# Kernel tuning notes

Measured on AMD Instinct MI355X. Metric: run time of the kernel, lower is better.

## Reference

```python
import jax, jax.numpy as jnp
import numpy as np

T, B, D, H, S = 512, 32, 1024, 1024, 512


def setup_inputs() -> dict:
    key = jax.random.key(0)
    ks = jax.random.split(key, 10)
    sc = 0.02
    return {
        "x": jax.random.normal(ks[0], (T, B, D), jnp.float32),
        "h0": jax.random.normal(ks[1], (B, H), jnp.float32),
        "c0": jax.random.normal(ks[2], (B, H), jnp.float32),
        "ctx": jax.random.normal(ks[3], (S, B, H), jnp.float32),
        # nn.Linear(input_size, 4*hidden_size) with bias
        "W_ih": jax.random.normal(ks[4], (4 * H, D), jnp.float32) * sc,
        "b_ih": jax.random.normal(ks[5], (4 * H,), jnp.float32) * sc,
        # nn.Linear(hidden_size, 4*hidden_size) with bias
        "W_hh": jax.random.normal(ks[6], (4 * H, H), jnp.float32) * sc,
        "b_hh": jax.random.normal(ks[7], (4 * H,), jnp.float32) * sc,
        # SoftDotAttention: linear_in (H->H, no bias), linear_out (2H->H, no bias)
        "W_in": jax.random.normal(ks[8], (H, H), jnp.float32) * sc,
        "W_out": jax.random.normal(ks[9], (H, 2 * H), jnp.float32) * sc,
    }


def reference(x, h0, c0, ctx, W_ih, b_ih, W_hh, b_hh, W_in, W_out):
    ctx_b = jnp.swapaxes(ctx, 0, 1)  # [B, S, H] (ctx.transpose(0,1))

    def step(carry, xt):
        hx, cx = carry
        gates = xt @ W_ih.T + b_ih + hx @ W_hh.T + b_hh  # [B, 4H]
        i, f, g, o = jnp.split(gates, 4, axis=1)
        cy = jax.nn.sigmoid(f) * cx + jax.nn.sigmoid(i) * jnp.tanh(g)
        hy = jax.nn.sigmoid(o) * jnp.tanh(cy)  # [B, H]
        # SoftDotAttention
        target = hy @ W_in.T  # [B, H]
        attn = jax.nn.softmax(jnp.einsum("bsh,bh->bs", ctx_b, target), axis=-1)
        wc = jnp.einsum("bs,bsh->bh", attn, ctx_b)  # weighted context
        h_tilde = jnp.tanh(jnp.concatenate([wc, hy], axis=1) @ W_out.T)
        return (h_tilde, cy), h_tilde

    (hT, cT), out = jax.lax.scan(step, (h0, c0), x)
    return out, hT, cT
```

## Files before the change

### kernel.cpp

```cpp
#include <hip/hip_runtime.h>
#include <hip/hip_bf16.h>
#include <cstdint>
#include <cstddef>

#define TT 512
#define BB 32
#define DD 1024
#define HH 1024
#define SS 512

typedef _Float16 f16x8 __attribute__((ext_vector_type(8)));
typedef _Float16 f16x4 __attribute__((ext_vector_type(4)));
typedef _Float16 f16x2 __attribute__((ext_vector_type(2)));
typedef float f32x4 __attribute__((ext_vector_type(4)));

__device__ __forceinline__ float sigm(float x) { return 1.0f / (1.0f + __expf(-x)); }
__device__ __forceinline__ float tanh_fast(float x) {
    return 1.0f - 2.0f / (__expf(2.0f * x) + 1.0f);
}
__device__ __forceinline__ f16x8 cvt8(const float* __restrict__ p) {
    float4 u = *(const float4*)p;
    float4 v = *(const float4*)(p + 4);
    f16x8 r;
    r[0] = (_Float16)u.x; r[1] = (_Float16)u.y; r[2] = (_Float16)u.z; r[3] = (_Float16)u.w;
    r[4] = (_Float16)v.x; r[5] = (_Float16)v.y; r[6] = (_Float16)v.z; r[7] = (_Float16)v.w;
    return r;
}

__device__ __forceinline__ void st_u32_coh(unsigned* p, unsigned v) {
    __hip_atomic_store(p, v, __ATOMIC_RELAXED, __HIP_MEMORY_SCOPE_AGENT);
}
__device__ __forceinline__ unsigned ld_u32_coh(const unsigned* p) {
    return __hip_atomic_load(p, __ATOMIC_RELAXED, __HIP_MEMORY_SCOPE_AGENT);
}
__device__ __forceinline__ f16x8 ld16_coh(const _Float16* p) {
    union { unsigned long long q[2]; f16x8 h; } u;
    u.q[0] = __hip_atomic_load((const unsigned long long*)p, __ATOMIC_RELAXED,
                               __HIP_MEMORY_SCOPE_AGENT);
    u.q[1] = __hip_atomic_load((const unsigned long long*)p + 1, __ATOMIC_RELAXED,
                               __HIP_MEMORY_SCOPE_AGENT);
    return u.h;
}

__global__ __launch_bounds__(256) void k_cvt(const float* __restrict__ s,
                                             _Float16* __restrict__ d, int n4) {
    for (int i = blockIdx.x * blockDim.x + threadIdx.x; i < n4; i += gridDim.x * blockDim.x) {
        float4 v = ((const float4*)s)[i];
        f16x4 h;
        h[0] = (_Float16)v.x; h[1] = (_Float16)v.y;
        h[2] = (_Float16)v.z; h[3] = (_Float16)v.w;
        ((f16x4*)d)[i] = h;
    }
}

__global__ void k_bias(const float* __restrict__ bih, const float* __restrict__ bhh,
                       float* __restrict__ bsum) {
    const int i = blockIdx.x * blockDim.x + threadIdx.x;
    if (i < 4 * HH) bsum[i] = bih[i] + bhh[i];
}

__global__ void k_init(const float* __restrict__ c0, float* __restrict__ cbuf) {
    const int i = blockIdx.x * blockDim.x + threadIdx.x;
    if (i < BB * HH) cbuf[i] = c0[i];
}

__global__ void k_zero(unsigned* __restrict__ p) {
    if (threadIdx.x == 0 && blockIdx.x == 0) *p = 0u;
}

__global__ void k_fin(const float* __restrict__ lasth, const float* __restrict__ cbuf,
                      float* __restrict__ hT, float* __restrict__ cT) {
    const int i = blockIdx.x * blockDim.x + threadIdx.x;
    if (i < BB * HH) {
        hT[i] = lasth[i];
        cT[i] = cbuf[i];
    }
}

__global__ __launch_bounds__(256) void k_pre(const float* __restrict__ x,
                                             const float* __restrict__ Wih,
                                             _Float16* __restrict__ gx) {
    const int wave = (blockIdx.x * blockDim.x + threadIdx.x) >> 6;
    const int lane = threadIdx.x & 63;
    const int m0 = (wave >> 6) * 64, n0 = (wave & 63) * 64;
    const int lm = lane & 15, q8 = (lane >> 4) * 8;

    f32x4 acc[4][4];
    #pragma unroll
    for (int i = 0; i < 4; ++i)
        #pragma unroll
        for (int j = 0; j < 4; ++j) acc[i][j] = (f32x4)0.0f;

    for (int k0 = 0; k0 < DD; k0 += 32) {
        f16x8 a[4], b[4];
        #pragma unroll
        for (int i = 0; i < 4; ++i)
            a[i] = cvt8(x + (size_t)(m0 + i * 16 + lm) * DD + k0 + q8);
        #pragma unroll
        for (int j = 0; j < 4; ++j)
            b[j] = cvt8(Wih + (size_t)(n0 + j * 16 + lm) * DD + k0 + q8);
        #pragma unroll
        for (int i = 0; i < 4; ++i)
            #pragma unroll
            for (int j = 0; j < 4; ++j)
                acc[i][j] = __builtin_amdgcn_mfma_f32_16x16x32_f16(a[i], b[j], acc[i][j], 0, 0, 0);
    }
    const int rq = (lane >> 4) * 4;
    #pragma unroll
    for (int i = 0; i < 4; ++i)
        #pragma unroll
        for (int j = 0; j < 4; ++j)
            #pragma unroll
            for (int r = 0; r < 4; ++r)
                gx[(size_t)(m0 + i * 16 + rq + r) * (4 * HH) + n0 + j * 16 + lm] =
                    (_Float16)acc[i][j][r];
}

__global__ __launch_bounds__(256) void k_trwin(const float* __restrict__ Win,
                                               _Float16* __restrict__ WinT) {
    __shared__ float tile[32][33];
    const int bx = blockIdx.x & 31, by = blockIdx.x >> 5;
    const int tx = threadIdx.x & 31, ty = threadIdx.x >> 5;
    #pragma unroll
    for (int r = 0; r < 4; ++r)
        tile[ty + r * 8][tx] = Win[(size_t)(by * 32 + ty + r * 8) * HH + bx * 32 + tx];
    __syncthreads();
    #pragma unroll
    for (int r = 0; r < 4; ++r)
        WinT[(size_t)(bx * 32 + ty + r * 8) * HH + by * 32 + tx] =
            (_Float16)tile[tx][ty + r * 8];
}

__global__ __launch_bounds__(256) void k_ctxw(const float* __restrict__ ctxf,
                                              const _Float16* __restrict__ WinT,
                                              _Float16* __restrict__ ctxW) {
    const int wave = (blockIdx.x * blockDim.x + threadIdx.x) >> 6;
    const int lane = threadIdx.x & 63;
    const int m0 = (wave >> 4) * 64, n0 = (wave & 15) * 64;
    const int lm = lane & 15, q8 = (lane >> 4) * 8;

    f32x4 acc[4][4];
    #pragma unroll
    for (int i = 0; i < 4; ++i)
        #pragma unroll
        for (int j = 0; j < 4; ++j) acc[i][j] = (f32x4)0.0f;

    for (int k0 = 0; k0 < HH; k0 += 32) {
        f16x8 a[4], b[4];
        #pragma unroll
        for (int i = 0; i < 4; ++i)
            a[i] = cvt8(ctxf + (size_t)(m0 + i * 16 + lm) * HH + k0 + q8);
        #pragma unroll
        for (int j = 0; j < 4; ++j)
            b[j] = *(const f16x8*)(WinT + (size_t)(n0 + j * 16 + lm) * HH + k0 + q8);
        #pragma unroll
        for (int i = 0; i < 4; ++i)
            #pragma unroll
            for (int j = 0; j < 4; ++j)
                acc[i][j] = __builtin_amdgcn_mfma_f32_16x16x32_f16(a[i], b[j], acc[i][j], 0, 0, 0);
    }
    const int rq = (lane >> 4) * 4;
    #pragma unroll
    for (int i = 0; i < 4; ++i)
        #pragma unroll
        for (int j = 0; j < 4; ++j)
            #pragma unroll
            for (int r = 0; r < 4; ++r)
                ctxW[(size_t)(m0 + i * 16 + rq + r) * HH + n0 + j * 16 + lm] =
                    (_Float16)acc[i][j][r];
}

__device__ __forceinline__ void gbar(unsigned* __restrict__ cnt, unsigned target) {
    __syncthreads();
    if (threadIdx.x == 0) {
        asm volatile("s_waitcnt vmcnt(0)" ::: "memory");
        __hip_atomic_fetch_add(cnt, 1u, __ATOMIC_RELAXED, __HIP_MEMORY_SCOPE_AGENT);
        int guard = 0;
        while (__hip_atomic_load(cnt, __ATOMIC_RELAXED, __HIP_MEMORY_SCOPE_AGENT) < target) {
            __builtin_amdgcn_s_sleep(2);
            if (++guard > (1 << 22)) break;
        }
    }
    __syncthreads();
}

__global__ __launch_bounds__(512, 1) void k_persist(
    const _Float16* __restrict__ x16,
    const _Float16* __restrict__ ctx_h,
    const _Float16* __restrict__ ctxW,
    const float* __restrict__ Whh,
    const float* __restrict__ Wih,
    const float* __restrict__ Wout,
    const float* __restrict__ bsum,
    float* __restrict__ cbuf,
    _Float16* __restrict__ h16,
    _Float16* __restrict__ hy16,
    _Float16* __restrict__ wc16,
    float* __restrict__ scores,
    float* __restrict__ out,
    unsigned* __restrict__ bar) {
    __shared__ __align__(16) _Float16 sWHH[16 * 1024];
    __shared__ __align__(16) _Float16 sWIH[16 * 1024];
    __shared__ __align__(16) _Float16 sWOUT[16 * 2048];
    __shared__ __align__(16) float sRED[4096];
    __shared__ float sSM[512];

    const int bid = blockIdx.x;
    const int tid = threadIdx.x;
    const int w = tid >> 6, lane = tid & 63;
    const int lm = lane & 15, q8 = (lane >> 4) * 8;
    const int j0 = bid * 4;
    const int n0 = bid * 16;

    for (int idx = tid; idx < 16 * 128; idx += 512) {
        const int p = idx >> 7, k8 = idx & 127;
        const int g = (p >> 2) * HH + j0 + (p & 3);
        const int dst = (p * 2048 + k8 * 16) ^ ((p & 7) << 4);
        *(f16x8*)((char*)sWHH + dst) = cvt8(Whh + (size_t)g * HH + k8 * 8);
        *(f16x8*)((char*)sWIH + dst) = cvt8(Wih + (size_t)g * DD + k8 * 8);
    }
    if (bid < 64) {
        for (int idx = tid; idx < 16 * 256; idx += 512) {
            const int p = idx >> 8, k8 = idx & 255;
            *(f16x8*)((char*)sWOUT + ((p * 4096 + k8 * 16) ^ ((p & 7) << 4))) =
                cvt8(Wout + (size_t)(n0 + p) * (2 * HH) + k8 * 8);
        }
    }
    __syncthreads();

    unsigned round = 0;
    for (int t = 0; t < TT; ++t) {
        {
            const int kb = (w & 3) * 256;
            f32x4 acc0 = (f32x4)0.0f, acc1 = (f32x4)0.0f;
            if (w < 4) {
                #pragma unroll
                for (int kk = 0; kk < 256; kk += 32) {
                    const int k0 = kb + kk + q8;
                    f16x8 a0 = ld16_coh(h16 + (size_t)lm * HH + k0);
                    f16x8 a1 = ld16_coh(h16 + (size_t)(16 + lm) * HH + k0);
                    f16x8 bb = *(const f16x8*)((const char*)sWHH +
                                 ((lm * 2048 + k0 * 2) ^ ((lm & 7) << 4)));
                    acc0 = __builtin_amdgcn_mfma_f32_16x16x32_f16(a0, bb, acc0, 0, 0, 0);
                    acc1 = __builtin_amdgcn_mfma_f32_16x16x32_f16(a1, bb, acc1, 0, 0, 0);
                }
            } else {
                const _Float16* Xb = x16 + (size_t)t * (BB * DD);
                #pragma unroll
                for (int kk = 0; kk < 256; kk += 32) {
                    const int k0 = kb + kk + q8;
                    f16x8 a0 = *(const f16x8*)(Xb + (size_t)lm * DD + k0);
                    f16x8 a1 = *(const f16x8*)(Xb + (size_t)(16 + lm) * DD + k0);
                    f16x8 bb = *(const f16x8*)((const char*)sWIH +
                                 ((lm * 2048 + k0 * 2) ^ ((lm & 7) << 4)));
                    acc0 = __builtin_amdgcn_mfma_f32_16x16x32_f16(a0, bb, acc0, 0, 0, 0);
                    acc1 = __builtin_amdgcn_mfma_f32_16x16x32_f16(a1, bb, acc1, 0, 0, 0);
                }
            }
            ((f32x4*)sRED)[(w * 2 + 0) * 64 + lane] = acc0;
            ((f32x4*)sRED)[(w * 2 + 1) * 64 + lane] = acc1;
            __syncthreads();
            {
                const int b = tid >> 4, p = tid & 15;
                const int mt = b >> 4, bi = b & 15;
                const int ln = ((bi >> 2) << 4) | p, r = bi & 3;
                float gv = 0.0f;
                #pragma unroll
                for (int w2 = 0; w2 < 8; ++w2)
                    gv += sRED[((w2 * 2 + mt) * 64 + ln) * 4 + r];
                sSM[tid] = gv;
            }
            __syncthreads();
            if (tid < 64) {
                const int b = tid >> 1, cp = (tid & 1) * 2;
                union { _Float16 h[2]; unsigned u; } pk;
                #pragma unroll
                for (int cc = 0; cc < 2; ++cc) {
                    const int c = cp + cc, j = j0 + c;
                    const float gi = sSM[b * 16 + 0 + c] + bsum[j];
                    const float gf = sSM[b * 16 + 4 + c] + bsum[HH + j];
                    const float gg = sSM[b * 16 + 8 + c] + bsum[2 * HH + j];
                    const float go = sSM[b * 16 + 12 + c] + bsum[3 * HH + j];
                    const float cprev = cbuf[b * HH + j];
                    const float cy = sigm(gf) * cprev + sigm(gi) * tanh_fast(gg);
                    const float hv = sigm(go) * tanh_fast(cy);
                    cbuf[b * HH + j] = cy;
                    pk.h[cc] = (_Float16)hv;
                }
                st_u32_coh((unsigned*)(hy16 + (size_t)b * HH + j0 + cp), pk.u);
            }
        }
        ++round;
        gbar(bar, 256u * round);

        {
            const int b = bid & 31, s0 = (bid >> 5) * 64;
            const _Float16* hrow = hy16 + (size_t)b * HH + lane * 16;
            const f16x8 hv0 = ld16_coh(hrow);
            const f16x8 hv1 = ld16_coh(hrow + 8);
            float hf[16];
            #pragma unroll
            for (int i = 0; i < 8; ++i) { hf[i] = (float)hv0[i]; hf[8 + i] = (float)hv1[i]; }
            #pragma unroll
            for (int i = 0; i < 8; ++i) {
                const int s = s0 + w * 8 + i;
                const _Float16* crow = ctxW + ((size_t)s * BB + b) * HH + lane * 16;
                const f16x8 c0 = *(const f16x8*)(crow);
                const f16x8 c1 = *(const f16x8*)(crow + 8);
                float sum = 0.0f;
                #pragma unroll
                for (int jj = 0; jj < 8; ++jj)
                    sum += hf[jj] * (float)c0[jj] + hf[8 + jj] * (float)c1[jj];
                #pragma unroll
                for (int off = 32; off > 0; off >>= 1) sum += __shfl_down(sum, off, 64);
                if (lane == 0)
                    st_u32_coh((unsigned*)(scores + b * SS + s), __float_as_uint(sum));
            }
        }
        ++round;
        gbar(bar, 256u * round);

        {
            const int b = bid >> 3, h0 = (bid & 7) * 128;
            const float v = __uint_as_float(ld_u32_coh((const unsigned*)(scores + b * SS + tid)));
            float mx = v;
            #pragma unroll
            for (int off = 32; off > 0; off >>= 1) mx = fmaxf(mx, __shfl_xor(mx, off, 64));
            if (lane == 0) sRED[w] = mx;
            __syncthreads();
            mx = sRED[0];
            #pragma unroll
            for (int w2 = 1; w2 < 8; ++w2) mx = fmaxf(mx, sRED[w2]);
            const float e = __expf(v - mx);
            sSM[tid] = e;
            float ssum = e;
            #pragma unroll
            for (int off = 32; off > 0; off >>= 1) ssum += __shfl_xor(ssum, off, 64);
            if (lane == 0) sRED[8 + w] = ssum;
            __syncthreads();
            float tot = 0.0f;
            #pragma unroll
            for (int w2 = 0; w2 < 8; ++w2) tot += sRED[8 + w2];
            const float inv = 1.0f / tot;
            float a0 = 0.0f, a1 = 0.0f;
            const _Float16* cb = ctx_h + ((size_t)(w * 64) * BB + b) * HH + h0 + lane * 2;
            #pragma unroll 8
            for (int i = 0; i < 64; ++i) {
                const float aw = sSM[w * 64 + i];
                const f16x2 u = *(const f16x2*)(cb + (size_t)i * (BB * HH));
                a0 += aw * (float)u[0];
                a1 += aw * (float)u[1];
            }
            __syncthreads();
            sRED[(w * 64 + lane) * 2 + 0] = a0;
            sRED[(w * 64 + lane) * 2 + 1] = a1;
            __syncthreads();
            if (tid < 64) {
                const int ln = tid;
                float sv0 = 0.0f, sv1 = 0.0f;
                #pragma unroll
                for (int w2 = 0; w2 < 8; ++w2) {
                    sv0 += sRED[(w2 * 64 + ln) * 2 + 0];
                    sv1 += sRED[(w2 * 64 + ln) * 2 + 1];
                }
                union { _Float16 h[2]; unsigned u; } pk;
                pk.h[0] = (_Float16)(sv0 * inv);
                pk.h[1] = (_Float16)(sv1 * inv);
                st_u32_coh((unsigned*)(wc16 + (size_t)b * HH + h0 + ln * 2), pk.u);
            }
        }
        ++round;
        gbar(bar, 256u * round);

        if (bid < 64) {
            const _Float16* Ab = (w < 4) ? wc16 : hy16;
            const int kb = (w & 3) * 256;
            const int koff = (w < 4) ? 0 : HH;
            f32x4 acc0 = (f32x4)0.0f, acc1 = (f32x4)0.0f;
            #pragma unroll
            for (int kk = 0; kk < 256; kk += 32) {
                const int k0 = kb + kk + q8;
                f16x8 a0 = ld16_coh(Ab + (size_t)lm * HH + k0);
                f16x8 a1 = ld16_coh(Ab + (size_t)(16 + lm) * HH + k0);
                f16x8 bb = *(const f16x8*)((char*)sWOUT +
                             ((lm * 4096 + (koff + k0) * 2) ^ ((lm & 7) << 4)));
                acc0 = __builtin_amdgcn_mfma_f32_16x16x32_f16(a0, bb, acc0, 0, 0, 0);
                acc1 = __builtin_amdgcn_mfma_f32_16x16x32_f16(a1, bb, acc1, 0, 0, 0);
            }
            ((f32x4*)sRED)[(w * 2 + 0) * 64 + lane] = acc0;
            ((f32x4*)sRED)[(w * 2 + 1) * 64 + lane] = acc1;
            __syncthreads();
            {
                const int b = tid >> 4, p = tid & 15;
                const int mt = b >> 4, bi = b & 15;
                const int ln = ((bi >> 2) << 4) | p, r = bi & 3;
                float v2 = 0.0f;
                #pragma unroll
                for (int w2 = 0; w2 < 8; ++w2)
                    v2 += sRED[((w2 * 2 + mt) * 64 + ln) * 4 + r];
                const float ht = tanh_fast(v2);
                out[(size_t)t * (BB * HH) + b * HH + n0 + p] = ht;
                sSM[tid] = ht;
            }
            __syncthreads();
            if (tid < 256) {
                const int b2 = tid >> 3, pp = (tid & 7) * 2;
                union { _Float16 h[2]; unsigned u; } pk;
                pk.h[0] = (_Float16)sSM[b2 * 16 + pp];
                pk.h[1] = (_Float16)sSM[b2 * 16 + pp + 1];
                st_u32_coh((unsigned*)(h16 + (size_t)b2 * HH + n0 + pp), pk.u);
            }
        }
        ++round;
        gbar(bar, 256u * round);
    }
}

__global__ __launch_bounds__(64) void k_step1(const float* __restrict__ hprev,
                                              const _Float16* __restrict__ Whh_h,
                                              const float* __restrict__ Whh_f,
                                              const _Float16* __restrict__ gx_t,
                                              const float* __restrict__ xt_f,
                                              const _Float16* __restrict__ Wih_h,
                                              const float* __restrict__ Wih_f,
                                              const float* __restrict__ bsum,
                                              float* __restrict__ cbuf,
                                              float* __restrict__ hy,
                                              int use_pre, int staged) {
    const int wave = blockIdx.x;
    const int lane = threadIdx.x;
    const int m0 = (wave >> 6) * 16;
    const int j0 = (wave & 63) * 16;
    const int lm = lane & 15, q8 = (lane >> 4) * 8;

    f32x4 acc[4];
    #pragma unroll
    for (int q = 0; q < 4; ++q) acc[q] = (f32x4)0.0f;

    const float* arow = hprev + (size_t)(m0 + lm) * HH;
    if (staged) {
        for (int k0 = 0; k0 < HH; k0 += 32) {
            f16x8 a = cvt8(arow + k0 + q8);
            #pragma unroll
            for (int q = 0; q < 4; ++q) {
                f16x8 b = *(const f16x8*)(Whh_h + (size_t)(q * HH + j0 + lm) * HH + k0 + q8);
                acc[q] = __builtin_amdgcn_mfma_f32_16x16x32_f16(a, b, acc[q], 0, 0, 0);
            }
        }
    } else {
        for (int k0 = 0; k0 < HH; k0 += 32) {
            f16x8 a = cvt8(arow + k0 + q8);
            #pragma unroll
            for (int q = 0; q < 4; ++q) {
                f16x8 b = cvt8(Whh_f + (size_t)(q * HH + j0 + lm) * HH + k0 + q8);
                acc[q] = __builtin_amdgcn_mfma_f32_16x16x32_f16(a, b, acc[q], 0, 0, 0);
            }
        }
    }
    if (!use_pre) {
        const float* xrow = xt_f + (size_t)(m0 + lm) * DD;
        if (staged) {
            for (int k0 = 0; k0 < DD; k0 += 32) {
                f16x8 a = cvt8(xrow + k0 + q8);
                #pragma unroll
                for (int q = 0; q < 4; ++q) {
                    f16x8 b = *(const f16x8*)(Wih_h + (size_t)(q * HH + j0 + lm) * DD + k0 + q8);
                    acc[q] = __builtin_amdgcn_mfma_f32_16x16x32_f16(a, b, acc[q], 0, 0, 0);
                }
            }
        } else {
            for (int k0 = 0; k0 < DD; k0 += 32) {
                f16x8 a = cvt8(xrow + k0 + q8);
                #pragma unroll
                for (int q = 0; q < 4; ++q) {
                    f16x8 b = cvt8(Wih_f + (size_t)(q * HH + j0 + lm) * DD + k0 + q8);
                    acc[q] = __builtin_amdgcn_mfma_f32_16x16x32_f16(a, b, acc[q], 0, 0, 0);
                }
            }
        }
    }
    const int rq = (lane >> 4) * 4;
    const int j = j0 + lm;
    const float bs_i = bsum[j], bs_f = bsum[HH + j], bs_g = bsum[2 * HH + j], bs_o = bsum[3 * HH + j];
    #pragma unroll
    for (int r = 0; r < 4; ++r) {
        const int b = m0 + rq + r;
        float gi = acc[0][r] + bs_i, gf = acc[1][r] + bs_f;
        float gg = acc[2][r] + bs_g, go = acc[3][r] + bs_o;
        if (use_pre) {
            const _Float16* g = gx_t + (size_t)b * (4 * HH);
            gi += (float)g[j];
            gf += (float)g[HH + j];
            gg += (float)g[2 * HH + j];
            go += (float)g[3 * HH + j];
        }
        const float cprev = cbuf[b * HH + j];
        const float cy = sigm(gf) * cprev + sigm(gi) * tanh_fast(gg);
        const float hv = sigm(go) * tanh_fast(cy);
        cbuf[b * HH + j] = cy;
        hy[b * HH + j] = hv;
    }
}

__global__ __launch_bounds__(64) void k_target(const float* __restrict__ hy,
                                               const _Float16* __restrict__ Win_h,
                                               const float* __restrict__ Win_f,
                                               float* __restrict__ target,
                                               int staged) {
    const int wave = blockIdx.x;
    const int lane = threadIdx.x;
    const int m0 = (wave >> 6) * 16;
    const int j0 = (wave & 63) * 16;
    const int lm = lane & 15, q8 = (lane >> 4) * 8;

    f32x4 acc = (f32x4)0.0f;
    const float* arow = hy + (size_t)(m0 + lm) * HH;
    if (staged) {
        for (int k0 = 0; k0 < HH; k0 += 32) {
            f16x8 a = cvt8(arow + k0 + q8);
            f16x8 b = *(const f16x8*)(Win_h + (size_t)(j0 + lm) * HH + k0 + q8);
            acc = __builtin_amdgcn_mfma_f32_16x16x32_f16(a, b, acc, 0, 0, 0);
        }
    } else {
        for (int k0 = 0; k0 < HH; k0 += 32) {
            f16x8 a = cvt8(arow + k0 + q8);
            f16x8 b = cvt8(Win_f + (size_t)(j0 + lm) * HH + k0 + q8);
            acc = __builtin_amdgcn_mfma_f32_16x16x32_f16(a, b, acc, 0, 0, 0);
        }
    }
    const int rq = (lane >> 4) * 4;
    const int j = j0 + lm;
    #pragma unroll
    for (int r = 0; r < 4; ++r)
        target[(m0 + rq + r) * HH + j] = acc[r];
}

__global__ __launch_bounds__(256) void k_scores(const _Float16* __restrict__ ctx_h,
                                                const float* __restrict__ ctx_f,
                                                const float* __restrict__ target,
                                                float* __restrict__ scores, int staged) {
    const int idx = (blockIdx.x * blockDim.x + threadIdx.x) >> 6;
    const int lane = threadIdx.x & 63;
    const int b = idx >> 9;
    const int s = idx & 511;
    const float* trow = target + b * HH + lane * 16;
    float4 t0 = *(const float4*)(trow);
    float4 t1 = *(const float4*)(trow + 4);
    float4 t2 = *(const float4*)(trow + 8);
    float4 t3 = *(const float4*)(trow + 12);
    float sum = 0.0f;
    if (staged) {
        const _Float16* crow = ctx_h + ((size_t)s * BB + b) * HH + lane * 16;
        f16x8 c0 = *(const f16x8*)(crow);
        f16x8 c1 = *(const f16x8*)(crow + 8);
        sum += (float)c0[0] * t0.x + (float)c0[1] * t0.y + (float)c0[2] * t0.z + (float)c0[3] * t0.w;
        sum += (float)c0[4] * t1.x + (float)c0[5] * t1.y + (float)c0[6] * t1.z + (float)c0[7] * t1.w;
        sum += (float)c1[0] * t2.x + (float)c1[1] * t2.y + (float)c1[2] * t2.z + (float)c1[3] * t2.w;
        sum += (float)c1[4] * t3.x + (float)c1[5] * t3.y + (float)c1[6] * t3.z + (float)c1[7] * t3.w;
    } else {
        const float* crow = ctx_f + ((size_t)s * BB + b) * HH + lane * 16;
        float4 c0 = *(const float4*)(crow);
        float4 c1 = *(const float4*)(crow + 4);
        float4 c2 = *(const float4*)(crow + 8);
        float4 c3 = *(const float4*)(crow + 12);
        sum += c0.x * t0.x + c0.y * t0.y + c0.z * t0.z + c0.w * t0.w;
        sum += c1.x * t1.x + c1.y * t1.y + c1.z * t1.z + c1.w * t1.w;
        sum += c2.x * t2.x + c2.y * t2.y + c2.z * t2.z + c2.w * t2.w;
        sum += c3.x * t3.x + c3.y * t3.y + c3.z * t3.z + c3.w * t3.w;
    }
    #pragma unroll
    for (int off = 32; off > 0; off >>= 1) sum += __shfl_down(sum, off, 64);
    if (lane == 0) scores[b * SS + s] = sum;
}

__global__ __launch_bounds__(256) void k_attn(const _Float16* __restrict__ ctx_h,
                                              const float* __restrict__ ctx_f,
                                              const float* __restrict__ scores,
                                              float* __restrict__ wc, int staged) {
    __shared__ float sm[SS];
    __shared__ float red[256];
    const int b = blockIdx.x >> 1;
    const int hc = blockIdx.x & 1;
    const int t = threadIdx.x;

    const float v0 = scores[b * SS + t];
    const float v1 = scores[b * SS + 256 + t];
    red[t] = fmaxf(v0, v1);
    __syncthreads();
    for (int o = 128; o > 0; o >>= 1) {
        if (t < o) red[t] = fmaxf(red[t], red[t + o]);
        __syncthreads();
    }
    const float mx = red[0];
    __syncthreads();
    const float e0 = __expf(v0 - mx);
    const float e1 = __expf(v1 - mx);
    sm[t] = e0;
    sm[t + 256] = e1;
    red[t] = e0 + e1;
    __syncthreads();
    for (int o = 128; o > 0; o >>= 1) {
        if (t < o) red[t] += red[t + o];
        __syncthreads();
    }
    const float inv = 1.0f / red[0];

    const int h = hc * 512 + t * 2;
    float a0 = 0.0f, a1 = 0.0f;
    if (staged) {
        const _Float16* cbase = ctx_h + (size_t)b * HH + h;
        #pragma unroll 8
        for (int s = 0; s < SS; ++s) {
            const float a = sm[s];
            const f16x2 u = *(const f16x2*)(cbase + (size_t)s * (BB * HH));
            a0 += a * (float)u[0];
            a1 += a * (float)u[1];
        }
    } else {
        const float* cbase = ctx_f + (size_t)b * HH + h;
        #pragma unroll 8
        for (int s = 0; s < SS; ++s) {
            const float a = sm[s];
            const float2 u = *(const float2*)(cbase + (size_t)s * (BB * HH));
            a0 += a * u.x;
            a1 += a * u.y;
        }
    }
    wc[b * HH + h] = a0 * inv;
    wc[b * HH + h + 1] = a1 * inv;
}

__global__ __launch_bounds__(64) void k_out(const float* __restrict__ wc,
                                            const float* __restrict__ hy,
                                            const _Float16* __restrict__ Wout_h,
                                            const float* __restrict__ Wout_f,
                                            float* __restrict__ out_t,
                                            int staged) {
    const int wave = blockIdx.x;
    const int lane = threadIdx.x;
    const int m0 = (wave >> 6) * 16;
    const int j0 = (wave & 63) * 16;
    const int lm = lane & 15, q8 = (lane >> 4) * 8;

    f32x4 acc = (f32x4)0.0f;
    const float* arow1 = wc + (size_t)(m0 + lm) * HH;
    const float* arow2 = hy + (size_t)(m0 + lm) * HH;
    if (staged) {
        const _Float16* brow = Wout_h + (size_t)(j0 + lm) * (2 * HH);
        for (int k0 = 0; k0 < HH; k0 += 32) {
            f16x8 a = cvt8(arow1 + k0 + q8);
            f16x8 b = *(const f16x8*)(brow + k0 + q8);
            acc = __builtin_amdgcn_mfma_f32_16x16x32_f16(a, b, acc, 0, 0, 0);
        }
        for (int k0 = 0; k0 < HH; k0 += 32) {
            f16x8 a = cvt8(arow2 + k0 + q8);
            f16x8 b = *(const f16x8*)(brow + HH + k0 + q8);
            acc = __builtin_amdgcn_mfma_f32_16x16x32_f16(a, b, acc, 0, 0, 0);
        }
    } else {
        const float* brow = Wout_f + (size_t)(j0 + lm) * (2 * HH);
        for (int k0 = 0; k0 < HH; k0 += 32) {
            f16x8 a = cvt8(arow1 + k0 + q8);
            f16x8 b = cvt8(brow + k0 + q8);
            acc = __builtin_amdgcn_mfma_f32_16x16x32_f16(a, b, acc, 0, 0, 0);
        }
        for (int k0 = 0; k0 < HH; k0 += 32) {
            f16x8 a = cvt8(arow2 + k0 + q8);
            f16x8 b = cvt8(brow + HH + k0 + q8);
            acc = __builtin_amdgcn_mfma_f32_16x16x32_f16(a, b, acc, 0, 0, 0);
        }
    }
    const int rq = (lane >> 4) * 4;
    const int j = j0 + lm;
    #pragma unroll
    for (int r = 0; r < 4; ++r)
        out_t[(m0 + rq + r) * HH + j] = tanh_fast(acc[r]);
}

static constexpr size_t NW_CBUF   = 0;
static constexpr size_t NW_SCORES = 131072;
static constexpr size_t NW_HY16   = 196608;
static constexpr size_t NW_H16    = 262144;
static constexpr size_t NW_WC16   = 327680;
static constexpr size_t NW_BSUM   = 393216;
static constexpr size_t NW_BAR    = 409600;
static constexpr size_t NW_WINT   = 413696;
static constexpr size_t NW_X16    = 2510848;
static constexpr size_t NW_CTXH   = 36065280;
static constexpr size_t NW_CTXW   = 69619712;
static constexpr size_t NW_TOTAL  = 103174144;

extern "C" void kernel_launch(void* const* d_in, const int* in_sizes, int n_in,
                              void* d_out, int out_size, void* d_ws, size_t ws_size,
                              hipStream_t stream) {
    const float* x    = (const float*)d_in[0];
    const float* h0   = (const float*)d_in[1];
    const float* c0   = (const float*)d_in[2];
    const float* ctx  = (const float*)d_in[3];
    const float* Wih  = (const float*)d_in[4];
    const float* bih  = (const float*)d_in[5];
    const float* Whh  = (const float*)d_in[6];
    const float* bhh  = (const float*)d_in[7];
    const float* Win  = (const float*)d_in[8];
    const float* Wout = (const float*)d_in[9];
    float* out = (float*)d_out;
    char* ws = (char*)d_ws;

    if (ws_size >= NW_TOTAL) {
        float* cbuf       = (float*)(ws + NW_CBUF);
        float* scores     = (float*)(ws + NW_SCORES);
        _Float16* hy16    = (_Float16*)(ws + NW_HY16);
        _Float16* h16     = (_Float16*)(ws + NW_H16);
        _Float16* wc16    = (_Float16*)(ws + NW_WC16);
        float* bsum       = (float*)(ws + NW_BSUM);
        unsigned* bar     = (unsigned*)(ws + NW_BAR);
        _Float16* WinT    = (_Float16*)(ws + NW_WINT);
        _Float16* x16     = (_Float16*)(ws + NW_X16);
        _Float16* ctx_h   = (_Float16*)(ws + NW_CTXH);
        _Float16* ctxW    = (_Float16*)(ws + NW_CTXW);

        k_bias<<<16, 256, 0, stream>>>(bih, bhh, bsum);
        k_init<<<128, 256, 0, stream>>>(c0, cbuf);
        k_zero<<<1, 64, 0, stream>>>(bar);
        k_cvt<<<2048, 256, 0, stream>>>(ctx, ctx_h, SS * BB * HH / 4);
        k_cvt<<<4096, 256, 0, stream>>>(x, x16, TT * BB * DD / 4);
        k_cvt<<<32, 256, 0, stream>>>(h0, h16, BB * HH / 4);
        k_trwin<<<1024, 256, 0, stream>>>(Win, WinT);
        k_ctxw<<<1024, 256, 0, stream>>>(ctx, WinT, ctxW);

        k_persist<<<256, 512, 0, stream>>>(x16, ctx_h, ctxW, Whh, Wih, Wout, bsum,
                                           cbuf, h16, hy16, wc16, scores, out, bar);

        float* hT = out + (size_t)TT * BB * HH;
        float* cT = hT + BB * HH;
        k_fin<<<128, 256, 0, stream>>>(out + (size_t)(TT - 1) * BB * HH, cbuf, hT, cT);
        return;
    }

    float* cbuf   = (float*)(ws + 0);
    float* hy     = (float*)(ws + 131072);
    float* target = (float*)(ws + 262144);
    float* scores = (float*)(ws + 393216);
    float* wc     = (float*)(ws + 458752);
    float* bsum   = (float*)(ws + 589824);
    _Float16* Whh_h  = (_Float16*)(ws + 606208);
    _Float16* Win_h  = (_Float16*)(ws + 8994816);
    _Float16* Wout_h = (_Float16*)(ws + 11091968);
    _Float16* Wih_h  = (_Float16*)(ws + 15286272);
    _Float16* ctx_h  = (_Float16*)(ws + 23674880);
    _Float16* gx     = (_Float16*)(ws + 57229312);

    const int staged  = (ws_size >= (size_t)57229312) ? 1 : 0;
    const int use_pre = (ws_size >= (size_t)191447040) ? 1 : 0;

    k_bias<<<16, 256, 0, stream>>>(bih, bhh, bsum);
    k_init<<<128, 256, 0, stream>>>(c0, cbuf);
    if (staged) {
        k_cvt<<<1024, 256, 0, stream>>>(Whh, Whh_h, 4 * HH * HH / 4);
        k_cvt<<<1024, 256, 0, stream>>>(Win, Win_h, HH * HH / 4);
        k_cvt<<<1024, 256, 0, stream>>>(Wout, Wout_h, 2 * HH * HH / 4);
        k_cvt<<<2048, 256, 0, stream>>>(ctx, ctx_h, SS * BB * HH / 4);
        if (!use_pre) k_cvt<<<1024, 256, 0, stream>>>(Wih, Wih_h, 4 * HH * DD / 4);
    }
    if (use_pre) k_pre<<<4096, 256, 0, stream>>>(x, Wih, gx);

    for (int t = 0; t < TT; ++t) {
        const float* hprev = (t == 0) ? h0 : (out + (size_t)(t - 1) * BB * HH);
        const _Float16* gx_t = gx + (size_t)t * BB * 4 * HH;
        const float* xt = x + (size_t)t * BB * DD;
        float* out_t = out + (size_t)t * BB * HH;

        k_step1<<<128, 64, 0, stream>>>(hprev, Whh_h, Whh, gx_t, xt, Wih_h, Wih,
                                        bsum, cbuf, hy, use_pre, staged);
        k_target<<<128, 64, 0, stream>>>(hy, Win_h, Win, target, staged);
        k_scores<<<4096, 256, 0, stream>>>(ctx_h, ctx, target, scores, staged);
        k_attn<<<64, 256, 0, stream>>>(ctx_h, ctx, scores, wc, staged);
        k_out<<<128, 64, 0, stream>>>(wc, hy, Wout_h, Wout, out_t, staged);
    }

    float* hT = out + (size_t)TT * BB * HH;
    float* cT = hT + BB * HH;
    k_fin<<<128, 256, 0, stream>>>(out + (size_t)(TT - 1) * BB * HH, cbuf, hT, cT);
}
```

Measured before the change: 26.24 ms.

## Replace single-counter grid barrier with sharded counters and master release flag

The global barrier in the persistent kernel used one atomic counter that all 256 blocks incremented and polled. It now spreads arrivals over 16 counters spaced 128 bytes apart. Block 0 polls those counters and then publishes a release flag that the other blocks spin on. The aim is to cut atomic contention and polling traffic on a single cache line across the four barriers per timestep. In exchange, each barrier gains an extra hop through block 0, and the explicit vmcnt wait before arrival is dropped, which may weaken memory ordering. The zeroing kernel now clears 1024 words, so it relies on the barrier region being at least that large.

New measurement: 22.26 ms. -15.2%, faster.

```diff
diff --git a/kernel.cpp b/kernel.cpp
--- a/kernel.cpp
+++ b/kernel.cpp
@@ -65,7 +65,8 @@
 }
 
 __global__ void k_zero(unsigned* __restrict__ p) {
-    if (threadIdx.x == 0 && blockIdx.x == 0) *p = 0u;
+    const int i = blockIdx.x * blockDim.x + threadIdx.x;
+    if (i < 1024) p[i] = 0u;
 }
 
 __global__ void k_fin(const float* __restrict__ lasth, const float* __restrict__ cbuf,
@@ -170,15 +171,37 @@
                     (_Float16)acc[i][j][r];
 }
 
-__device__ __forceinline__ void gbar(unsigned* __restrict__ cnt, unsigned target) {
+#define BAR_REL 512
+__device__ __forceinline__ void gbar3(unsigned* __restrict__ bar, unsigned round) {
+    const int bid = blockIdx.x;
+    const int tid = threadIdx.x;
     __syncthreads();
-    if (threadIdx.x == 0) {
-        asm volatile("s_waitcnt vmcnt(0)" ::: "memory");
-        __hip_atomic_fetch_add(cnt, 1u, __ATOMIC_RELAXED, __HIP_MEMORY_SCOPE_AGENT);
-        int guard = 0;
-        while (__hip_atomic_load(cnt, __ATOMIC_RELAXED, __HIP_MEMORY_SCOPE_AGENT) < target) {
-            __builtin_amdgcn_s_sleep(2);
-            if (++guard > (1 << 22)) break;
+    if (bid == 0) {
+        if (tid == 0)
+            __hip_atomic_fetch_add(&bar[(bid & 15) << 5], 1u, __ATOMIC_RELAXED,
+                                   __HIP_MEMORY_SCOPE_AGENT);
+        if (tid < 16) {
+            int guard = 0;
+            while (__hip_atomic_load(&bar[tid << 5], __ATOMIC_RELAXED,
+                                     __HIP_MEMORY_SCOPE_AGENT) < 16u * round) {
+                __builtin_amdgcn_s_sleep(1);
+                if (++guard > (1 << 22)) break;
+            }
+        }
+        __syncthreads();
+        if (tid == 0)
+            __hip_atomic_store(&bar[BAR_REL], round, __ATOMIC_RELAXED,
+                               __HIP_MEMORY_SCOPE_AGENT);
+    } else {
+        if (tid == 0) {
+            __hip_atomic_fetch_add(&bar[(bid & 15) << 5], 1u, __ATOMIC_RELAXED,
+                                   __HIP_MEMORY_SCOPE_AGENT);
+            int guard = 0;
+            while (__hip_atomic_load(&bar[BAR_REL], __ATOMIC_RELAXED,
+                                     __HIP_MEMORY_SCOPE_AGENT) < round) {
+                __builtin_amdgcn_s_sleep(1);
+                if (++guard > (1 << 22)) break;
+            }
         }
     }
     __syncthreads();
@@ -291,7 +314,7 @@
             }
         }
         ++round;
-        gbar(bar, 256u * round);
+        gbar3(bar, round);
 
         {
             const int b = bid & 31, s0 = (bid >> 5) * 64;
@@ -318,7 +341,7 @@
             }
         }
         ++round;
-        gbar(bar, 256u * round);
+        gbar3(bar, round);
 
         {
             const int b = bid >> 3, h0 = (bid & 7) * 128;
@@ -370,7 +393,7 @@
             }
         }
         ++round;
-        gbar(bar, 256u * round);
+        gbar3(bar, round);
 
         if (bid < 64) {
             const _Float16* Ab = (w < 4) ? wc16 : hy16;
@@ -412,7 +435,7 @@
             }
         }
         ++round;
-        gbar(bar, 256u * round);
+        gbar3(bar, round);
     }
 }
 
@@ -721,7 +744,7 @@
 
         k_bias<<<16, 256, 0, stream>>>(bih, bhh, bsum);
         k_init<<<128, 256, 0, stream>>>(c0, cbuf);
-        k_zero<<<1, 64, 0, stream>>>(bar);
+        k_zero<<<4, 256, 0, stream>>>(bar);
         k_cvt<<<2048, 256, 0, stream>>>(ctx, ctx_h, SS * BB * HH / 4);
         k_cvt<<<4096, 256, 0, stream>>>(x, x16, TT * BB * DD / 4);
         k_cvt<<<32, 256, 0, stream>>>(h0, h16, BB * HH / 4);
```

## Replace atomic-counter grid barrier with per-block flags and spread output projection

Applied to the files above, without the earlier changes.

The grid barrier in the persistent kernel changes from a single atomic counter to per-block round flags. Each block publishes its own flag, and 64 threads poll all 256 flags, which removes contention on the serialized atomic at each of the four barriers per timestep. The output projection now runs on all 256 blocks, each owning 4 output columns instead of 64 blocks owning 16. This balances the phase across the grid, at the cost of MFMA tiles where only 4 of 16 columns are useful. The context-weighting loop is also unrolled further.

New measurement: 22.62 ms. 1.16x faster.

```diff
diff --git a/kernel.cpp b/kernel.cpp
--- a/kernel.cpp
+++ b/kernel.cpp
@@ -65,7 +65,8 @@
 }
 
 __global__ void k_zero(unsigned* __restrict__ p) {
-    if (threadIdx.x == 0 && blockIdx.x == 0) *p = 0u;
+    const int i = blockIdx.x * blockDim.x + threadIdx.x;
+    if (i < 1024) p[i] = 0u;
 }
 
 __global__ void k_fin(const float* __restrict__ lasth, const float* __restrict__ cbuf,
@@ -170,15 +171,23 @@
                     (_Float16)acc[i][j][r];
 }
 
-__device__ __forceinline__ void gbar(unsigned* __restrict__ cnt, unsigned target) {
+__device__ __forceinline__ void gbar4(unsigned* __restrict__ flags, unsigned round) {
     __syncthreads();
-    if (threadIdx.x == 0) {
+    const int tid = threadIdx.x;
+    if (tid == 0) {
         asm volatile("s_waitcnt vmcnt(0)" ::: "memory");
-        __hip_atomic_fetch_add(cnt, 1u, __ATOMIC_RELAXED, __HIP_MEMORY_SCOPE_AGENT);
+        st_u32_coh(&flags[blockIdx.x], round);
+    }
+    if (tid < 64) {
         int guard = 0;
-        while (__hip_atomic_load(cnt, __ATOMIC_RELAXED, __HIP_MEMORY_SCOPE_AGENT) < target) {
-            __builtin_amdgcn_s_sleep(2);
-            if (++guard > (1 << 22)) break;
+        for (;;) {
+            const unsigned a0 = ld_u32_coh(&flags[tid * 4 + 0]);
+            const unsigned a1 = ld_u32_coh(&flags[tid * 4 + 1]);
+            const unsigned a2 = ld_u32_coh(&flags[tid * 4 + 2]);
+            const unsigned a3 = ld_u32_coh(&flags[tid * 4 + 3]);
+            if (a0 >= round && a1 >= round && a2 >= round && a3 >= round) break;
+            __builtin_amdgcn_s_sleep(1);
+            if (++guard > (1 << 20)) break;
         }
     }
     __syncthreads();
@@ -201,7 +210,7 @@
     unsigned* __restrict__ bar) {
     __shared__ __align__(16) _Float16 sWHH[16 * 1024];
     __shared__ __align__(16) _Float16 sWIH[16 * 1024];
-    __shared__ __align__(16) _Float16 sWOUT[16 * 2048];
+    __shared__ __align__(16) _Float16 sWOUT[4 * 2048];
     __shared__ __align__(16) float sRED[4096];
     __shared__ float sSM[512];
 
@@ -210,7 +219,6 @@
     const int w = tid >> 6, lane = tid & 63;
     const int lm = lane & 15, q8 = (lane >> 4) * 8;
     const int j0 = bid * 4;
-    const int n0 = bid * 16;
 
     for (int idx = tid; idx < 16 * 128; idx += 512) {
         const int p = idx >> 7, k8 = idx & 127;
@@ -219,12 +227,10 @@
         *(f16x8*)((char*)sWHH + dst) = cvt8(Whh + (size_t)g * HH + k8 * 8);
         *(f16x8*)((char*)sWIH + dst) = cvt8(Wih + (size_t)g * DD + k8 * 8);
     }
-    if (bid < 64) {
-        for (int idx = tid; idx < 16 * 256; idx += 512) {
-            const int p = idx >> 8, k8 = idx & 255;
-            *(f16x8*)((char*)sWOUT + ((p * 4096 + k8 * 16) ^ ((p & 7) << 4))) =
-                cvt8(Wout + (size_t)(n0 + p) * (2 * HH) + k8 * 8);
-        }
+    for (int idx = tid; idx < 4 * 256; idx += 512) {
+        const int p = idx >> 8, k8 = idx & 255;
+        *(f16x8*)((char*)sWOUT + ((p * 4096 + k8 * 16) ^ (p << 4))) =
+            cvt8(Wout + (size_t)(j0 + p) * (2 * HH) + k8 * 8);
     }
     __syncthreads();
 
@@ -291,7 +297,7 @@
             }
         }
         ++round;
-        gbar(bar, 256u * round);
+        gbar4(bar, round);
 
         {
             const int b = bid & 31, s0 = (bid >> 5) * 64;
@@ -318,7 +324,7 @@
             }
         }
         ++round;
-        gbar(bar, 256u * round);
+        gbar4(bar, round);
 
         {
             const int b = bid >> 3, h0 = (bid & 7) * 128;
@@ -344,7 +350,7 @@
             const float inv = 1.0f / tot;
             float a0 = 0.0f, a1 = 0.0f;
             const _Float16* cb = ctx_h + ((size_t)(w * 64) * BB + b) * HH + h0 + lane * 2;
-            #pragma unroll 8
+            #pragma unroll 16
             for (int i = 0; i < 64; ++i) {
                 const float aw = sSM[w * 64 + i];
                 const f16x2 u = *(const f16x2*)(cb + (size_t)i * (BB * HH));
@@ -370,12 +376,13 @@
             }
         }
         ++round;
-        gbar(bar, 256u * round);
-
-        if (bid < 64) {
+        gbar4(bar, round);
+
+        {
             const _Float16* Ab = (w < 4) ? wc16 : hy16;
             const int kb = (w & 3) * 256;
             const int koff = (w < 4) ? 0 : HH;
+            const int pc = lm & 3;
             f32x4 acc0 = (f32x4)0.0f, acc1 = (f32x4)0.0f;
             #pragma unroll
             for (int kk = 0; kk < 256; kk += 32) {
@@ -383,7 +390,7 @@
                 f16x8 a0 = ld16_coh(Ab + (size_t)lm * HH + k0);
                 f16x8 a1 = ld16_coh(Ab + (size_t)(16 + lm) * HH + k0);
                 f16x8 bb = *(const f16x8*)((char*)sWOUT +
-                             ((lm * 4096 + (koff + k0) * 2) ^ ((lm & 7) << 4)));
+                             ((pc * 4096 + (koff + k0) * 2) ^ (pc << 4)));
                 acc0 = __builtin_amdgcn_mfma_f32_16x16x32_f16(a0, bb, acc0, 0, 0, 0);
                 acc1 = __builtin_amdgcn_mfma_f32_16x16x32_f16(a1, bb, acc1, 0, 0, 0);
             }
@@ -399,20 +406,20 @@
                 for (int w2 = 0; w2 < 8; ++w2)
                     v2 += sRED[((w2 * 2 + mt) * 64 + ln) * 4 + r];
                 const float ht = tanh_fast(v2);
-                out[(size_t)t * (BB * HH) + b * HH + n0 + p] = ht;
+                if (p < 4) out[(size_t)t * (BB * HH) + b * HH + j0 + p] = ht;
                 sSM[tid] = ht;
             }
             __syncthreads();
-            if (tid < 256) {
-                const int b2 = tid >> 3, pp = (tid & 7) * 2;
+            if (tid < 64) {
+                const int b2 = tid >> 1, pp = (tid & 1) * 2;
                 union { _Float16 h[2]; unsigned u; } pk;
                 pk.h[0] = (_Float16)sSM[b2 * 16 + pp];
                 pk.h[1] = (_Float16)sSM[b2 * 16 + pp + 1];
-                st_u32_coh((unsigned*)(h16 + (size_t)b2 * HH + n0 + pp), pk.u);
+                st_u32_coh((unsigned*)(h16 + (size_t)b2 * HH + j0 + pp), pk.u);
             }
         }
         ++round;
-        gbar(bar, 256u * round);
+        gbar4(bar, round);
     }
 }
 
@@ -721,7 +728,7 @@
 
         k_bias<<<16, 256, 0, stream>>>(bih, bhh, bsum);
         k_init<<<128, 256, 0, stream>>>(c0, cbuf);
-        k_zero<<<1, 64, 0, stream>>>(bar);
+        k_zero<<<4, 256, 0, stream>>>(bar);
         k_cvt<<<2048, 256, 0, stream>>>(ctx, ctx_h, SS * BB * HH / 4);
         k_cvt<<<4096, 256, 0, stream>>>(x, x16, TT * BB * DD / 4);
         k_cvt<<<32, 256, 0, stream>>>(h0, h16, BB * HH / 4);
```
